# Kernel tuning notes

Hardware: AMD Instinct MI355X
Metric: run time of the kernel (lower is better)

## Reference

```python
import jax, jax.numpy as jnp
import numpy as np

V, E, H, L = 50000, 300, 256, 5
B, T_C, T_T = 64, 637, 24


def _lstm_dir(x, wih, whh, b, reverse):
    # x: [B,T,E]; wih: [4H,E]; whh: [4H,H]; b: [4H]
    pre = jnp.einsum('bte,ge->btg', x, wih) + b  # [B,T,4H]
    h0 = jnp.zeros((x.shape[0], whh.shape[1]), x.dtype)

    def step(carry, p):
        h, c = carry
        g = p + h @ whh.T
        i, f, gg, o = jnp.split(g, 4, axis=-1)
        c = jax.nn.sigmoid(f) * c + jax.nn.sigmoid(i) * jnp.tanh(gg)
        h = jax.nn.sigmoid(o) * jnp.tanh(c)
        return (h, c), h

    _, hs = jax.lax.scan(step, (h0, h0), jnp.swapaxes(pre, 0, 1), reverse=reverse)
    return jnp.swapaxes(hs, 0, 1)  # [B,T,H]


def _bilstm(x, wih_f, whh_f, b_f, wih_b, whh_b, b_b):
    return jnp.concatenate([
        _lstm_dir(x, wih_f, whh_f, b_f, False),
        _lstm_dir(x, wih_b, whh_b, b_b, True),
    ], axis=-1)  # [B,T,2H]


def setup_inputs() -> dict:
    key = jax.random.key(0)
    ks = jax.random.split(key, 20)
    k = 1.0 / np.sqrt(H)
    u = lambda kk, shape: jax.random.uniform(kk, shape, jnp.float32, -k, k)
    inp = {
        'content': jax.random.randint(ks[0], (B, T_C), 0, V),
        'title': jax.random.randint(ks[1], (B, T_T), 0, V),
        'embed_w': jax.random.normal(ks[2], (V, E), jnp.float32),
        't_wih_f': u(ks[3], (4 * H, E)), 't_whh_f': u(ks[4], (4 * H, H)), 't_b_f': u(ks[5], (4 * H,)),
        't_wih_b': u(ks[6], (4 * H, E)), 't_whh_b': u(ks[7], (4 * H, H)), 't_b_b': u(ks[8], (4 * H,)),
        'c_wih_f': u(ks[9], (4 * H, E)), 'c_whh_f': u(ks[10], (4 * H, H)), 'c_b_f': u(ks[11], (4 * H,)),
        'c_wih_b': u(ks[12], (4 * H, E)), 'c_whh_b': u(ks[13], (4 * H, H)), 'c_b_b': u(ks[14], (4 * H,)),
        'att_w': u(ks[15], (2 * H, 2 * H)),
        'fc_w': u(ks[16], (L, T_C)), 'fc_b': u(ks[17], (L,)),
    }
    return inp


def reference(content, title, embed_w, t_wih_f, t_whh_f, t_b_f, t_wih_b, t_whh_b, t_b_b,
              c_wih_f, c_whh_f, c_b_f, c_wih_b, c_whh_b, c_b_b, att_w, fc_w, fc_b):
    content_embed = embed_w[content]  # [B,Tc,E]
    title_embed = embed_w[title]      # [B,Tt,E]
    title_rep = _bilstm(title_embed, t_wih_f, t_whh_f, t_b_f, t_wih_b, t_whh_b, t_b_b)
    content_rep = _bilstm(content_embed, c_wih_f, c_whh_f, c_b_f, c_wih_b, c_whh_b, c_b_b)
    title_last = title_rep[:, -1, :]  # [B,2H]
    # score[b,t] = title_last[b] . (att_w @ content_rep[b,t])  (Linear with weight att_w: x @ att_w.T)
    a = jnp.einsum('bj,jk,btk->bt', title_last, att_w, content_rep)  # [B,Tc]
    a = jax.nn.softmax(a, axis=1)
    return jax.nn.log_softmax(a @ fc_w.T + fc_b, axis=1)  # [B,L]
```

## Files before the change

kernel.cpp:

```cpp
#include <hip/hip_runtime.h>
#include <stdint.h>

typedef __attribute__((ext_vector_type(8))) short bf16x8v;
typedef __attribute__((ext_vector_type(4))) float f32x4v;
typedef long long i64;
typedef __attribute__((ext_vector_type(2))) long long i64x2;

#define DEV static __device__ __forceinline__

#define B_   64
#define TC_  637
#define TCP_ 638
#define TT_  24
#define E_   300
#define KP_  320
#define H_   256
#define NG_  2048

DEV uint16_t f2bf(float f) {
    uint32_t u = __float_as_uint(f);
    u += 0x7fffu + ((u >> 16) & 1u);
    return (uint16_t)(u >> 16);
}
DEV float bf2f(uint16_t h) { return __uint_as_float(((uint32_t)h) << 16); }

DEV void gload_lds16(const void* g, void* l) {
    __builtin_amdgcn_global_load_lds((const __attribute__((address_space(1))) uint32_t*)g,
                                     (__attribute__((address_space(3))) uint32_t*)l, 16, 0, 0);
}

__global__ void k_pg(const float* t_wih_f, const float* t_wih_b,
                     const float* t_whh_f,
                     const float* c_wih_f, const float* c_wih_b,
                     const float* c_whh_f, const float* c_whh_b,
                     const float* t_b_f, const float* t_b_b,
                     const float* c_b_f, const float* c_b_b,
                     uint16_t* BwC, uint16_t* BwT, float* biasC, float* biasT,
                     uint32_t* w8CF, uint32_t* w8CB, uint32_t* w8TF,
                     const int* __restrict__ content, const int* __restrict__ title,
                     const float* __restrict__ emb,
                     uint16_t* __restrict__ Ac, uint16_t* __restrict__ At)
{
    if (blockIdx.x < 256) {
        int tid = blockIdx.x*blockDim.x + threadIdx.x;
        int nth = 256*256;
        for (int i = tid; i < NG_*KP_; i += nth) {
            int n = i / KP_, k = i - n*KP_;
            float vc = 0.f, vt = 0.f;
            if (k < E_) {
                vc = (n < 1024) ? c_wih_f[n*E_+k] : c_wih_b[(n-1024)*E_+k];
                vt = (n < 1024) ? t_wih_f[n*E_+k] : t_wih_b[(n-1024)*E_+k];
            }
            BwC[i] = f2bf(vc); BwT[i] = f2bf(vt);
        }
        for (int i = tid; i < 1024*H_/4; i += nth) {
            int base = i*4;
            uint32_t a, b, c;
            a = (uint32_t)__builtin_amdgcn_cvt_pk_fp8_f32(c_whh_f[base], c_whh_f[base+1], 0, false);
            a = (uint32_t)__builtin_amdgcn_cvt_pk_fp8_f32(c_whh_f[base+2], c_whh_f[base+3], (int)a, true);
            b = (uint32_t)__builtin_amdgcn_cvt_pk_fp8_f32(c_whh_b[base], c_whh_b[base+1], 0, false);
            b = (uint32_t)__builtin_amdgcn_cvt_pk_fp8_f32(c_whh_b[base+2], c_whh_b[base+3], (int)b, true);
            c = (uint32_t)__builtin_amdgcn_cvt_pk_fp8_f32(t_whh_f[base], t_whh_f[base+1], 0, false);
            c = (uint32_t)__builtin_amdgcn_cvt_pk_fp8_f32(t_whh_f[base+2], t_whh_f[base+3], (int)c, true);
            w8CF[i] = a; w8CB[i] = b; w8TF[i] = c;
        }
        for (int i = tid; i < NG_; i += nth) {
            biasC[i] = (i < 1024) ? c_b_f[i] : c_b_b[i-1024];
            biasT[i] = (i < 1024) ? t_b_f[i] : t_b_b[i-1024];
        }
    } else {
        int tid = (blockIdx.x - 256)*blockDim.x + threadIdx.x;
        int nth = 2048*256;
        const int CCH = 40832*40;
        const int TCH = 1536*40;
        for (int i = tid; i < CCH + TCH; i += nth) {
            uint16_t* dst; int row, c8; int tok;
            if (i < CCH) {
                row = i / 40; c8 = i - row*40;
                int t = row >> 6, b = row & 63;
                tok = (t < TC_) ? content[b*TC_ + t] : -1;
                dst = Ac + (size_t)row*KP_ + c8*8;
            } else {
                int jx = i - CCH;
                row = jx / 40; c8 = jx - row*40;
                int t = row >> 6, b = row & 63;
                tok = title[b*TT_ + t];
                dst = At + (size_t)row*KP_ + c8*8;
            }
            uint32_t dd[4];
            #pragma unroll
            for (int p = 0; p < 4; ++p) {
                int k = c8*8 + p*2;
                float f0 = (tok >= 0 && k   < E_) ? emb[(size_t)tok*E_ + k]   : 0.f;
                float f1 = (tok >= 0 && k+1 < E_) ? emb[(size_t)tok*E_ + k+1] : 0.f;
                dd[p] = (uint32_t)f2bf(f0) | ((uint32_t)f2bf(f1) << 16);
            }
            uint4 q; q.x = dd[0]; q.y = dd[1]; q.z = dd[2]; q.w = dd[3];
            *(uint4*)dst = q;
        }
    }
}

__global__ __launch_bounds__(256) void k_gemm(const uint16_t* __restrict__ A,
        const uint16_t* __restrict__ Bw, const float* __restrict__ bias,
        uint16_t* __restrict__ prep,
        const uint16_t* __restrict__ A2, const uint16_t* __restrict__ Bw2,
        const float* __restrict__ bias2, uint16_t* __restrict__ prep2)
{
    __shared__ __align__(16) uint16_t lA[2][128*32];
    __shared__ __align__(16) uint16_t lB[2][128*32];
    const int tid = threadIdx.x;
    const int l = tid & 63, wv = tid >> 6;

    const uint16_t* Ax; const uint16_t* Bx; const float* bx; uint16_t* px; int m0;
    if (blockIdx.y < 319) { Ax = A;  Bx = Bw;  bx = bias;  px = prep;  m0 = blockIdx.y*128; }
    else                  { Ax = A2; Bx = Bw2; bx = bias2; px = prep2; m0 = (blockIdx.y-319)*128; }
    const int n0 = blockIdx.x * 128;

    auto stage = [&](int kc, int bi) {
        #pragma unroll
        for (int r = 0; r < 2; ++r) {
            int row = r*64 + (tid >> 2);
            int cu  = (tid & 3) * 8;
            gload_lds16(Ax + (size_t)(m0 + row)*KP_ + kc*32 + cu, &lA[bi][r*2048 + wv*512]);
            gload_lds16(Bx + (size_t)(n0 + row)*KP_ + kc*32 + cu, &lB[bi][r*2048 + wv*512]);
        }
    };

    f32x4v acc[4][4];
    #pragma unroll
    for (int i = 0; i < 4; ++i)
        #pragma unroll
        for (int j = 0; j < 4; ++j)
            acc[i][j] = f32x4v{0.f,0.f,0.f,0.f};

    const int mtb = (wv >> 1) * 4, ntb = (wv & 1) * 4;

    stage(0, 0);
    __syncthreads();
    for (int kc = 0; kc < 10; ++kc) {
        if (kc < 9) stage(kc + 1, (kc + 1) & 1);
        {
            int bi = kc & 1;
            bf16x8v af[4], bfr[4];
            #pragma unroll
            for (int i = 0; i < 4; ++i) {
                af[i]  = *(const bf16x8v*)&lA[bi][((mtb+i)*16 + (l&15))*32 + (l>>4)*8];
                bfr[i] = *(const bf16x8v*)&lB[bi][((ntb+i)*16 + (l&15))*32 + (l>>4)*8];
            }
            #pragma unroll
            for (int i = 0; i < 4; ++i)
                #pragma unroll
                for (int j = 0; j < 4; ++j)
                    acc[i][j] = __builtin_amdgcn_mfma_f32_16x16x32_bf16(bfr[j], af[i], acc[i][j], 0,0,0);
        }
        __syncthreads();
    }

    const int hi = l >> 4;
    #pragma unroll
    for (int j = 0; j < 4; ++j) {
        int n16 = (n0 >> 4) + ntb + j;
        int dir = n16 >> 6;
        int q   = n16 & 63;
        int ty  = q >> 4;
        int wp  = q & 15;
        float4 bv = *(const float4*)(bx + n16*16 + hi*4);
        #pragma unroll
        for (int i = 0; i < 4; ++i) {
            int rowblk = (m0 >> 4) + mtb + i;
            int t    = rowblk >> 2;
            int bblk = rowblk & 3;
            int unit = t*8 + bblk*2 + dir;
            ushort4 pk;
            pk.x = f2bf(acc[i][j][0] + bv.x);
            pk.y = f2bf(acc[i][j][1] + bv.y);
            pk.z = f2bf(acc[i][j][2] + bv.z);
            pk.w = f2bf(acc[i][j][3] + bv.w);
            size_t off = (size_t)unit*16384 + (size_t)wp*1024 + (size_t)l*16 + ty*4;
            *(ushort4*)(px + off) = pk;
        }
    }
}

#define MF(ACC, W, AA) asm("v_mfma_f32_16x16x32_fp8_fp8 %0, %1, %2, %0" \
                           : "+v"(ACC) : "a"(W), "v"(AA))

__global__ __launch_bounds__(1024, 4) void k_rnn(
    const uint16_t* __restrict__ preC, const uint16_t* __restrict__ preT,
    const uint8_t* __restrict__ w8CF, const uint8_t* __restrict__ w8CB,
    const uint8_t* __restrict__ w8TF,
    uint16_t* __restrict__ cr, float* __restrict__ tl)
{
    __shared__ __align__(16) char smem[8192];

    const int tid = threadIdx.x;
    const int l = tid & 63, wp = tid >> 6;
    const int m = l & 15, hi = l >> 4;
    const int u = blockIdx.x;

    int dir, bblk, t0, tstep, nsteps, tlOff = -1;
    bool doCR = false;
    const uint16_t* pre; const uint8_t* whh8 = nullptr;
    if (u < 8) {
        dir = u & 1; bblk = u >> 1;
        nsteps = TC_; t0 = dir ? (TC_-1) : 0; tstep = dir ? -1 : 1;
        whh8 = dir ? w8CB : w8CF; pre = preC; doCR = true;
    } else if (u < 12) {
        dir = 0; bblk = u - 8; nsteps = TT_; t0 = 0; tstep = 1;
        whh8 = w8TF; pre = preT; tlOff = 0;
    } else {
        dir = 1; bblk = u - 12; nsteps = 1; t0 = TT_-1; tstep = -1;
        whh8 = nullptr; pre = preT; tlOff = 256;
    }
    const int b0 = bblk * 16;

    i64 w8r[4][8];
    if (whh8) {
        #pragma unroll
        for (int ty = 0; ty < 4; ++ty) {
            int n = ty*256 + wp*16 + m;
            #pragma unroll
            for (int kc = 0; kc < 8; ++kc)
                w8r[ty][kc] = *(const i64*)(whh8 + (size_t)n*H_ + kc*32 + hi*8);
        }
        #pragma unroll
        for (int ty = 0; ty < 4; ++ty)
            #pragma unroll
            for (int kc = 0; kc < 8; ++kc)
                asm volatile("" : "+a"(w8r[ty][kc]));
    }
    for (int i = tid; i < 2048; i += 1024) ((uint32_t*)smem)[i] = 0;
    __syncthreads();

    int rda[4];
    #pragma unroll
    for (int q = 0; q < 4; ++q) rda[q] = m*256 + hi*64 + (((q ^ (m & 3))) << 4);
    const int waddr = m*256 + (((wp*2 + (hi >> 1)) & 3) << 6)
                    + ((((wp >> 2) ^ (m & 3))) << 4)
                    + (((wp >> 1) & 1) << 3) + ((hi & 1) << 2);

    uint16_t* crp = cr + ((size_t)(b0 + m)*TC_ + t0)*512 + dir*256 + (wp << 4) + hi*4;
    const intptr_t crAdv = (intptr_t)tstep * 512;

    float cst[4] = {0.f, 0.f, 0.f, 0.f};

    const uint16_t* pp = pre + (size_t)(t0*8 + bblk*2 + dir)*16384
                             + (size_t)(wp << 10) + (size_t)l*16;
    const intptr_t ppAdv = (intptr_t)tstep * 131072;

    uint4 pf0 = *(const uint4*)(pp);
    uint4 pf1 = *(const uint4*)(pp + 8);

    const float KN = -1.4426950408889634f;
    const float K2 =  2.8853900817779268f;

    for (int s = 0; s < nsteps; ++s) {
        const char* hb = (const char*)smem + (s & 1)*4096;
        char*       ho = smem + ((s & 1) ^ 1)*4096;

        f32x4v acc[4];
        acc[0][0]=__uint_as_float(pf0.x<<16); acc[0][1]=__uint_as_float(pf0.x&0xffff0000u);
        acc[0][2]=__uint_as_float(pf0.y<<16); acc[0][3]=__uint_as_float(pf0.y&0xffff0000u);
        acc[1][0]=__uint_as_float(pf0.z<<16); acc[1][1]=__uint_as_float(pf0.z&0xffff0000u);
        acc[1][2]=__uint_as_float(pf0.w<<16); acc[1][3]=__uint_as_float(pf0.w&0xffff0000u);
        acc[2][0]=__uint_as_float(pf1.x<<16); acc[2][1]=__uint_as_float(pf1.x&0xffff0000u);
        acc[2][2]=__uint_as_float(pf1.y<<16); acc[2][3]=__uint_as_float(pf1.y&0xffff0000u);
        acc[3][0]=__uint_as_float(pf1.z<<16); acc[3][1]=__uint_as_float(pf1.z&0xffff0000u);
        acc[3][2]=__uint_as_float(pf1.w<<16); acc[3][3]=__uint_as_float(pf1.w&0xffff0000u);

        if (s + 1 < nsteps) {
            pp += ppAdv;
            pf0 = *(const uint4*)(pp);
            pf1 = *(const uint4*)(pp + 8);
        }

        if (whh8) {
            __builtin_amdgcn_s_setprio(1);
            #pragma unroll
            for (int q = 0; q < 4; ++q) {
                i64x2 a = *(const i64x2*)(hb + rda[q]);
                MF(acc[0], w8r[0][2*q], a[0]);
                MF(acc[1], w8r[1][2*q], a[0]);
                MF(acc[2], w8r[2][2*q], a[0]);
                MF(acc[3], w8r[3][2*q], a[0]);
                MF(acc[0], w8r[0][2*q+1], a[1]);
                MF(acc[1], w8r[1][2*q+1], a[1]);
                MF(acc[2], w8r[2][2*q+1], a[1]);
                MF(acc[3], w8r[3][2*q+1], a[1]);
            }
            __builtin_amdgcn_s_setprio(0);
        }

        float hv[4];
        #pragma unroll
        for (int r = 0; r < 4; ++r) {
            float Ei = __builtin_amdgcn_exp2f(acc[0][r] * KN);
            float Ef = __builtin_amdgcn_exp2f(acc[1][r] * KN);
            float Eg = __builtin_amdgcn_exp2f(acc[2][r] * (2.f*KN));
            float Eo = __builtin_amdgcn_exp2f(acc[3][r] * KN);
            float A  = 1.f + Ei;
            float Bb = 1.f + Eg;
            float C  = 1.f + Ef;
            float AB = A * Bb;
            float num = __builtin_fmaf(cst[r], AB, (2.f - Bb) * C);
            float cv  = num * __builtin_amdgcn_rcpf(AB * C);
            cst[r] = cv;
            float cc = fminf(fmaxf(cv, -15.f), 15.f);
            float P  = __builtin_amdgcn_exp2f(cc * K2);
            hv[r] = (P - 1.f) * __builtin_amdgcn_rcpf((1.f + Eo) * (P + 1.f));
        }

        uint32_t p8 = (uint32_t)__builtin_amdgcn_cvt_pk_fp8_f32(hv[0], hv[1], 0, false);
        p8 = (uint32_t)__builtin_amdgcn_cvt_pk_fp8_f32(hv[2], hv[3], (int)p8, true);
        *(uint32_t*)(ho + waddr) = p8;

        if (doCR) {
            uint32_t b01, b23;
            asm("v_cvt_pk_bf16_f32 %0, %1, %2" : "=v"(b01) : "v"(hv[0]), "v"(hv[1]));
            asm("v_cvt_pk_bf16_f32 %0, %1, %2" : "=v"(b23) : "v"(hv[2]), "v"(hv[3]));
            uint2 st; st.x = b01; st.y = b23;
            *(uint2*)crp = st;
            crp += crAdv;
        }
        if (tlOff >= 0 && s == nsteps - 1) {
            float4 fv; fv.x = hv[0]; fv.y = hv[1]; fv.z = hv[2]; fv.w = hv[3];
            *(float4*)(tl + (size_t)(b0 + m)*512 + tlOff + (wp << 4) + hi*4) = fv;
        }

        __builtin_amdgcn_sched_barrier(0);
        asm volatile("s_waitcnt lgkmcnt(0)" ::: "memory");
        __builtin_amdgcn_s_barrier();
        __builtin_amdgcn_sched_barrier(0);
    }
}

__global__ __launch_bounds__(256) void k_attn(const uint16_t* __restrict__ cr,
        const float* __restrict__ tl, const float* __restrict__ attw,
        const float* __restrict__ fcw, const float* __restrict__ fcb,
        float* __restrict__ out)
{
    __shared__ float sT[512];
    __shared__ float sQ[512];
    __shared__ float sS[640];
    __shared__ float sR[256];
    const int b = blockIdx.x, tid = threadIdx.x;
    for (int i = tid; i < 512; i += 256) sT[i] = tl[(size_t)b*512 + i];
    __syncthreads();
    for (int n = tid; n < 512; n += 256) {
        float s = 0.f;
        for (int j = 0; j < 512; ++j) s += sT[j] * attw[(size_t)j*512 + n];
        sQ[n] = s;
    }
    __syncthreads();
    for (int t = tid; t < TC_; t += 256) {
        const uint16_t* row = cr + ((size_t)b*TC_ + t)*512;
        float s = 0.f;
        for (int c = 0; c < 64; ++c) {
            uint4 v = *(const uint4*)(row + c*8);
            uint32_t d;
            d = v.x; s += bf2f((uint16_t)(d&0xffff))*sQ[c*8+0] + bf2f((uint16_t)(d>>16))*sQ[c*8+1];
            d = v.y; s += bf2f((uint16_t)(d&0xffff))*sQ[c*8+2] + bf2f((uint16_t)(d>>16))*sQ[c*8+3];
            d = v.z; s += bf2f((uint16_t)(d&0xffff))*sQ[c*8+4] + bf2f((uint16_t)(d>>16))*sQ[c*8+5];
            d = v.w; s += bf2f((uint16_t)(d&0xffff))*sQ[c*8+6] + bf2f((uint16_t)(d>>16))*sQ[c*8+7];
        }
        sS[t] = s;
    }
    __syncthreads();
    float lm = -1e30f;
    for (int t = tid; t < TC_; t += 256) lm = fmaxf(lm, sS[t]);
    sR[tid] = lm; __syncthreads();
    for (int o = 128; o > 0; o >>= 1) { if (tid < o) sR[tid] = fmaxf(sR[tid], sR[tid+o]); __syncthreads(); }
    float M = sR[0]; __syncthreads();
    float ls = 0.f;
    for (int t = tid; t < TC_; t += 256) { float e = __expf(sS[t]-M); sS[t] = e; ls += e; }
    sR[tid] = ls; __syncthreads();
    for (int o = 128; o > 0; o >>= 1) { if (tid < o) sR[tid] += sR[tid+o]; __syncthreads(); }
    float inv = 1.f / sR[0]; __syncthreads();
    float la[5] = {0.f,0.f,0.f,0.f,0.f};
    for (int t = tid; t < TC_; t += 256) {
        float p = sS[t] * inv;
        #pragma unroll
        for (int ll = 0; ll < 5; ++ll) la[ll] += p * fcw[ll*TC_ + t];
    }
    float lg[5];
    #pragma unroll
    for (int ll = 0; ll < 5; ++ll) {
        sR[tid] = la[ll]; __syncthreads();
        for (int o = 128; o > 0; o >>= 1) { if (tid < o) sR[tid] += sR[tid+o]; __syncthreads(); }
        lg[ll] = sR[0] + fcb[ll]; __syncthreads();
    }
    if (tid == 0) {
        float m2 = lg[0];
        #pragma unroll
        for (int ll = 1; ll < 5; ++ll) m2 = fmaxf(m2, lg[ll]);
        float se = 0.f;
        #pragma unroll
        for (int ll = 0; ll < 5; ++ll) se += __expf(lg[ll] - m2);
        float lse = __logf(se) + m2;
        #pragma unroll
        for (int ll = 0; ll < 5; ++ll) out[b*5 + ll] = lg[ll] - lse;
    }
}

extern "C" void kernel_launch(void* const* d_in, const int* in_sizes, int n_in,
                              void* d_out, int out_size, void* d_ws, size_t ws_size,
                              hipStream_t stream)
{
    const int*   content = (const int*)d_in[0];
    const int*   title   = (const int*)d_in[1];
    const float* embed_w = (const float*)d_in[2];
    const float* t_wih_f = (const float*)d_in[3];
    const float* t_whh_f = (const float*)d_in[4];
    const float* t_b_f   = (const float*)d_in[5];
    const float* t_wih_b = (const float*)d_in[6];
    const float* t_b_b   = (const float*)d_in[8];
    const float* c_wih_f = (const float*)d_in[9];
    const float* c_whh_f = (const float*)d_in[10];
    const float* c_b_f   = (const float*)d_in[11];
    const float* c_wih_b = (const float*)d_in[12];
    const float* c_whh_b = (const float*)d_in[13];
    const float* c_b_b   = (const float*)d_in[14];
    const float* att_w   = (const float*)d_in[15];
    const float* fc_w    = (const float*)d_in[16];
    const float* fc_b    = (const float*)d_in[17];
    float* out = (float*)d_out;

    char* ws = (char*)d_ws;
    size_t o = 0;
    auto alloc = [&](size_t sz) { char* p = ws + o; o = (o + sz + 255) & ~(size_t)255; return p; };
    uint16_t* Ac    = (uint16_t*)alloc((size_t)40832*KP_*2);
    uint16_t* At    = (uint16_t*)alloc((size_t)1536*KP_*2);
    uint16_t* BwC   = (uint16_t*)alloc((size_t)NG_*KP_*2);
    uint16_t* BwT   = (uint16_t*)alloc((size_t)NG_*KP_*2);
    float*    biasC = (float*)   alloc((size_t)NG_*4);
    float*    biasT = (float*)   alloc((size_t)NG_*4);
    uint8_t*  w8CF  = (uint8_t*) alloc((size_t)1024*H_);
    uint8_t*  w8CB  = (uint8_t*) alloc((size_t)1024*H_);
    uint8_t*  w8TF  = (uint8_t*) alloc((size_t)1024*H_);
    uint16_t* preC  = (uint16_t*)alloc((size_t)TCP_*262144);
    uint16_t* preT  = (uint16_t*)alloc((size_t)TT_*262144);
    uint16_t* crp   = (uint16_t*)alloc((size_t)B_*TC_*512*2);
    float*    tlp   = (float*)   alloc((size_t)B_*512*4);

    k_pg<<<2304, 256, 0, stream>>>(t_wih_f, t_wih_b, t_whh_f, c_wih_f, c_wih_b,
                                   c_whh_f, c_whh_b, t_b_f, t_b_b, c_b_f, c_b_b,
                                   BwC, BwT, biasC, biasT,
                                   (uint32_t*)w8CF, (uint32_t*)w8CB, (uint32_t*)w8TF,
                                   content, title, embed_w, Ac, At);
    k_gemm<<<dim3(16, 331), 256, 0, stream>>>(Ac, BwC, biasC, preC,
                                              At, BwT, biasT, preT);
    k_rnn<<<16, 1024, 0, stream>>>(preC, preT, w8CF, w8CB, w8TF, crp, tlp);
    k_attn<<<64, 256, 0, stream>>>(crp, tlp, att_w, fc_w, fc_b, out);
}
```

Baseline: 1.454 ms.

## Restructure LSTM recurrence to 512-thread blocks interleaving two batch chunks

```diff
diff --git a/kernel.cpp b/kernel.cpp
--- a/kernel.cpp
+++ b/kernel.cpp
@@ -164,7 +164,8 @@
         int dir = n16 >> 6;
         int q   = n16 & 63;
         int ty  = q >> 4;
-        int wp  = q & 15;
+        int wpx = q & 15;
+        int wp8 = wpx >> 1, ct = wpx & 1;
         float4 bv = *(const float4*)(bx + n16*16 + hi*4);
         #pragma unroll
         for (int i = 0; i < 4; ++i) {
@@ -177,7 +178,8 @@
             pk.y = f2bf(acc[i][j][1] + bv.y);
             pk.z = f2bf(acc[i][j][2] + bv.z);
             pk.w = f2bf(acc[i][j][3] + bv.w);
-            size_t off = (size_t)unit*16384 + (size_t)wp*1024 + (size_t)l*16 + ty*4;
+            size_t off = (size_t)unit*16384 + (size_t)wp8*2048 + (size_t)ct*1024
+                       + (size_t)l*16 + ty*4;
             *(ushort4*)(px + off) = pk;
         }
     }
@@ -186,146 +188,253 @@
 #define MF(ACC, W, AA) asm("v_mfma_f32_16x16x32_fp8_fp8 %0, %1, %2, %0" \
                            : "+v"(ACC) : "a"(W), "v"(AA))
 
-__global__ __launch_bounds__(1024, 4) void k_rnn(
+#define DEC(A0, A1, A2, A3)                                                          \
+  acc[0][0][0]=__uint_as_float(A0.x<<16); acc[0][0][1]=__uint_as_float(A0.x&0xffff0000u); \
+  acc[0][0][2]=__uint_as_float(A0.y<<16); acc[0][0][3]=__uint_as_float(A0.y&0xffff0000u); \
+  acc[1][0][0]=__uint_as_float(A0.z<<16); acc[1][0][1]=__uint_as_float(A0.z&0xffff0000u); \
+  acc[1][0][2]=__uint_as_float(A0.w<<16); acc[1][0][3]=__uint_as_float(A0.w&0xffff0000u); \
+  acc[2][0][0]=__uint_as_float(A1.x<<16); acc[2][0][1]=__uint_as_float(A1.x&0xffff0000u); \
+  acc[2][0][2]=__uint_as_float(A1.y<<16); acc[2][0][3]=__uint_as_float(A1.y&0xffff0000u); \
+  acc[3][0][0]=__uint_as_float(A1.z<<16); acc[3][0][1]=__uint_as_float(A1.z&0xffff0000u); \
+  acc[3][0][2]=__uint_as_float(A1.w<<16); acc[3][0][3]=__uint_as_float(A1.w&0xffff0000u); \
+  acc[0][1][0]=__uint_as_float(A2.x<<16); acc[0][1][1]=__uint_as_float(A2.x&0xffff0000u); \
+  acc[0][1][2]=__uint_as_float(A2.y<<16); acc[0][1][3]=__uint_as_float(A2.y&0xffff0000u); \
+  acc[1][1][0]=__uint_as_float(A2.z<<16); acc[1][1][1]=__uint_as_float(A2.z&0xffff0000u); \
+  acc[1][1][2]=__uint_as_float(A2.w<<16); acc[1][1][3]=__uint_as_float(A2.w&0xffff0000u); \
+  acc[2][1][0]=__uint_as_float(A3.x<<16); acc[2][1][1]=__uint_as_float(A3.x&0xffff0000u); \
+  acc[2][1][2]=__uint_as_float(A3.y<<16); acc[2][1][3]=__uint_as_float(A3.y&0xffff0000u); \
+  acc[3][1][0]=__uint_as_float(A3.z<<16); acc[3][1][1]=__uint_as_float(A3.z&0xffff0000u); \
+  acc[3][1][2]=__uint_as_float(A3.w<<16); acc[3][1][3]=__uint_as_float(A3.w&0xffff0000u);
+
+#define MFMA_BLOCK(HB)                                     \
+  __builtin_amdgcn_s_setprio(1);                           \
+  _Pragma("unroll")                                        \
+  for (int q = 0; q < 4; ++q) {                            \
+    i64x2 a = *(const i64x2*)((HB) + rda[q]);              \
+    MF(acc[0][0], w8r[0][0][2*q], a[0]);                   \
+    MF(acc[1][0], w8r[1][0][2*q], a[0]);                   \
+    MF(acc[2][0], w8r[2][0][2*q], a[0]);                   \
+    MF(acc[3][0], w8r[3][0][2*q], a[0]);                   \
+    MF(acc[0][1], w8r[0][1][2*q], a[0]);                   \
+    MF(acc[1][1], w8r[1][1][2*q], a[0]);                   \
+    MF(acc[2][1], w8r[2][1][2*q], a[0]);                   \
+    MF(acc[3][1], w8r[3][1][2*q], a[0]);                   \
+    MF(acc[0][0], w8r[0][0][2*q+1], a[1]);                 \
+    MF(acc[1][0], w8r[1][0][2*q+1], a[1]);                 \
+    MF(acc[2][0], w8r[2][0][2*q+1], a[1]);                 \
+    MF(acc[3][0], w8r[3][0][2*q+1], a[1]);                 \
+    MF(acc[0][1], w8r[0][1][2*q+1], a[1]);                 \
+    MF(acc[1][1], w8r[1][1][2*q+1], a[1]);                 \
+    MF(acc[2][1], w8r[2][1][2*q+1], a[1]);                 \
+    MF(acc[3][1], w8r[3][1][2*q+1], a[1]);                 \
+  }                                                        \
+  __builtin_amdgcn_s_setprio(0);
+
+#define NL(CT, CS, HV)                                                          \
+  _Pragma("unroll")                                                             \
+  for (int r = 0; r < 4; ++r) {                                                 \
+    float Ei = __builtin_amdgcn_exp2f(acc[0][CT][r] * KN);                      \
+    float Ef = __builtin_amdgcn_exp2f(acc[1][CT][r] * KN);                      \
+    float Eg = __builtin_amdgcn_exp2f(acc[2][CT][r] * (2.f*KN));                \
+    float Eo = __builtin_amdgcn_exp2f(acc[3][CT][r] * KN);                      \
+    float Av = 1.f + Ei, Bb = 1.f + Eg, Cv = 1.f + Ef;                          \
+    float AB = Av * Bb;                                                         \
+    float num = __builtin_fmaf(CS[r], AB, (2.f - Bb) * Cv);                     \
+    float cv  = num * __builtin_amdgcn_rcpf(AB * Cv);                           \
+    CS[r] = cv;                                                                 \
+    float cc = fminf(fmaxf(cv, -15.f), 15.f);                                   \
+    float P  = __builtin_amdgcn_exp2f(cc * K2);                                 \
+    HV[r] = (P - 1.f) * __builtin_amdgcn_rcpf((1.f + Eo) * (P + 1.f));          \
+  }
+
+__global__ __launch_bounds__(512, 2) void k_rnn(
     const uint16_t* __restrict__ preC, const uint16_t* __restrict__ preT,
     const uint8_t* __restrict__ w8CF, const uint8_t* __restrict__ w8CB,
     const uint8_t* __restrict__ w8TF,
     uint16_t* __restrict__ cr, float* __restrict__ tl)
 {
-    __shared__ __align__(16) char smem[8192];
+    __shared__ __align__(16) char smem[16384];
 
     const int tid = threadIdx.x;
-    const int l = tid & 63, wp = tid >> 6;
+    const int l = tid & 63, wp8 = tid >> 6;
     const int m = l & 15, hi = l >> 4;
     const int u = blockIdx.x;
 
-    int dir, bblk, t0, tstep, nsteps, tlOff = -1;
-    bool doCR = false;
-    const uint16_t* pre; const uint8_t* whh8 = nullptr;
-    if (u < 8) {
-        dir = u & 1; bblk = u >> 1;
-        nsteps = TC_; t0 = dir ? (TC_-1) : 0; tstep = dir ? -1 : 1;
-        whh8 = dir ? w8CB : w8CF; pre = preC; doCR = true;
-    } else if (u < 12) {
-        dir = 0; bblk = u - 8; nsteps = TT_; t0 = 0; tstep = 1;
-        whh8 = w8TF; pre = preT; tlOff = 0;
+    const float KN = -1.4426950408889634f;
+    const float K2 =  2.8853900817779268f;
+
+    if (u == 6) {
+        for (int chunk = 0; chunk < 4; ++chunk) {
+            const uint16_t* pp = preT + (size_t)((TT_-1)*8 + chunk*2 + 1)*16384
+                               + (size_t)wp8*2048 + (size_t)l*16;
+            uint4 p0 = *(const uint4*)(pp);
+            uint4 p1 = *(const uint4*)(pp + 8);
+            uint4 p2 = *(const uint4*)(pp + 1024);
+            uint4 p3 = *(const uint4*)(pp + 1032);
+            f32x4v acc[4][2];
+            DEC(p0, p1, p2, p3);
+            float cz0[4] = {0,0,0,0}, cz1[4] = {0,0,0,0};
+            float hv0[4], hv1[4];
+            NL(0, cz0, hv0);
+            NL(1, cz1, hv1);
+            float* tb = tl + (size_t)(chunk*16 + m)*512 + 256 + wp8*32 + hi*4;
+            float4 f0; f0.x=hv0[0]; f0.y=hv0[1]; f0.z=hv0[2]; f0.w=hv0[3];
+            float4 f1; f1.x=hv1[0]; f1.y=hv1[1]; f1.z=hv1[2]; f1.w=hv1[3];
+            *(float4*)tb = f0;
+            *(float4*)(tb + 16) = f1;
+        }
+        return;
+    }
+
+    int dir, nsteps, t0, tstep, tlOff, chunkA, chunkB;
+    bool doCR;
+    const uint16_t* pre; const uint8_t* whh8;
+    if (u < 4) {
+        dir = u >> 1; int pr = u & 1;
+        chunkA = pr*2; chunkB = pr*2 + 1;
+        nsteps = TC_; t0 = dir ? TC_-1 : 0; tstep = dir ? -1 : 1;
+        whh8 = dir ? w8CB : w8CF; pre = preC; doCR = true; tlOff = -1;
     } else {
-        dir = 1; bblk = u - 12; nsteps = 1; t0 = TT_-1; tstep = -1;
-        whh8 = nullptr; pre = preT; tlOff = 256;
-    }
-    const int b0 = bblk * 16;
-
-    i64 w8r[4][8];
-    if (whh8) {
-        #pragma unroll
-        for (int ty = 0; ty < 4; ++ty) {
-            int n = ty*256 + wp*16 + m;
+        dir = 0; int pr = u - 4;
+        chunkA = pr*2; chunkB = pr*2 + 1;
+        nsteps = TT_; t0 = 0; tstep = 1;
+        whh8 = w8TF; pre = preT; doCR = false; tlOff = 0;
+    }
+
+    i64 w8r[4][2][8];
+    #pragma unroll
+    for (int ty = 0; ty < 4; ++ty)
+        #pragma unroll
+        for (int ct = 0; ct < 2; ++ct) {
+            int n = ty*256 + wp8*32 + ct*16 + m;
             #pragma unroll
             for (int kc = 0; kc < 8; ++kc)
-                w8r[ty][kc] = *(const i64*)(whh8 + (size_t)n*H_ + kc*32 + hi*8);
-        }
-        #pragma unroll
-        for (int ty = 0; ty < 4; ++ty)
+                w8r[ty][ct][kc] = *(const i64*)(whh8 + (size_t)n*H_ + kc*32 + hi*8);
+        }
+    #pragma unroll
+    for (int ty = 0; ty < 4; ++ty)
+        #pragma unroll
+        for (int ct = 0; ct < 2; ++ct)
             #pragma unroll
             for (int kc = 0; kc < 8; ++kc)
-                asm volatile("" : "+a"(w8r[ty][kc]));
-    }
-    for (int i = tid; i < 2048; i += 1024) ((uint32_t*)smem)[i] = 0;
+                asm volatile("" : "+a"(w8r[ty][ct][kc]));
+
+    for (int i = tid; i < 4096; i += 512) ((uint32_t*)smem)[i] = 0;
     __syncthreads();
 
     int rda[4];
     #pragma unroll
-    for (int q = 0; q < 4; ++q) rda[q] = m*256 + hi*64 + (((q ^ (m & 3))) << 4);
-    const int waddr = m*256 + (((wp*2 + (hi >> 1)) & 3) << 6)
-                    + ((((wp >> 2) ^ (m & 3))) << 4)
-                    + (((wp >> 1) & 1) << 3) + ((hi & 1) << 2);
-
-    uint16_t* crp = cr + ((size_t)(b0 + m)*TC_ + t0)*512 + dir*256 + (wp << 4) + hi*4;
+    for (int q = 0; q < 4; ++q) rda[q] = m*256 + hi*64 + ((q ^ (m & 3)) << 4);
+    auto WAD = [&](int wpx) {
+        return m*256 + (((wpx*2 + (hi >> 1)) & 3) << 6)
+             + (((wpx >> 2) ^ (m & 3)) << 4)
+             + (((wpx >> 1) & 1) << 3) + ((hi & 1) << 2);
+    };
+    const int wA0 = WAD(wp8*2), wA1 = WAD(wp8*2 + 1);
+
+    uint16_t* crpA = cr + ((size_t)(chunkA*16 + m)*TC_ + t0)*512 + dir*256 + wp8*32 + hi*4;
+    uint16_t* crpB = cr + ((size_t)(chunkB*16 + m)*TC_ + t0)*512 + dir*256 + wp8*32 + hi*4;
     const intptr_t crAdv = (intptr_t)tstep * 512;
 
-    float cst[4] = {0.f, 0.f, 0.f, 0.f};
-
-    const uint16_t* pp = pre + (size_t)(t0*8 + bblk*2 + dir)*16384
-                             + (size_t)(wp << 10) + (size_t)l*16;
+    float cstA[2][4] = {{0,0,0,0},{0,0,0,0}};
+    float cstB[2][4] = {{0,0,0,0},{0,0,0,0}};
+
+    const uint16_t* ppA = pre + (size_t)(t0*8 + chunkA*2 + dir)*16384
+                        + (size_t)wp8*2048 + (size_t)l*16;
+    const uint16_t* ppB = pre + (size_t)(t0*8 + chunkB*2 + dir)*16384
+                        + (size_t)wp8*2048 + (size_t)l*16;
     const intptr_t ppAdv = (intptr_t)tstep * 131072;
 
-    uint4 pf0 = *(const uint4*)(pp);
-    uint4 pf1 = *(const uint4*)(pp + 8);
-
-    const float KN = -1.4426950408889634f;
-    const float K2 =  2.8853900817779268f;
+    uint4 pf0 = *(const uint4*)(ppA);
+    uint4 pf1 = *(const uint4*)(ppA + 8);
+    uint4 pf2 = *(const uint4*)(ppA + 1024);
+    uint4 pf3 = *(const uint4*)(ppA + 1032);
 
     for (int s = 0; s < nsteps; ++s) {
-        const char* hb = (const char*)smem + (s & 1)*4096;
-        char*       ho = smem + ((s & 1) ^ 1)*4096;
-
-        f32x4v acc[4];
-        acc[0][0]=__uint_as_float(pf0.x<<16); acc[0][1]=__uint_as_float(pf0.x&0xffff0000u);
-        acc[0][2]=__uint_as_float(pf0.y<<16); acc[0][3]=__uint_as_float(pf0.y&0xffff0000u);
-        acc[1][0]=__uint_as_float(pf0.z<<16); acc[1][1]=__uint_as_float(pf0.z&0xffff0000u);
-        acc[1][2]=__uint_as_float(pf0.w<<16); acc[1][3]=__uint_as_float(pf0.w&0xffff0000u);
-        acc[2][0]=__uint_as_float(pf1.x<<16); acc[2][1]=__uint_as_float(pf1.x&0xffff0000u);
-        acc[2][2]=__uint_as_float(pf1.y<<16); acc[2][3]=__uint_as_float(pf1.y&0xffff0000u);
-        acc[3][0]=__uint_as_float(pf1.z<<16); acc[3][1]=__uint_as_float(pf1.z&0xffff0000u);
-        acc[3][2]=__uint_as_float(pf1.w<<16); acc[3][3]=__uint_as_float(pf1.w&0xffff0000u);
-
-        if (s + 1 < nsteps) {
-            pp += ppAdv;
-            pf0 = *(const uint4*)(pp);
-            pf1 = *(const uint4*)(pp + 8);
-        }
-
-        if (whh8) {
-            __builtin_amdgcn_s_setprio(1);
-            #pragma unroll
-            for (int q = 0; q < 4; ++q) {
-                i64x2 a = *(const i64x2*)(hb + rda[q]);
-                MF(acc[0], w8r[0][2*q], a[0]);
-                MF(acc[1], w8r[1][2*q], a[0]);
-                MF(acc[2], w8r[2][2*q], a[0]);
-                MF(acc[3], w8r[3][2*q], a[0]);
-                MF(acc[0], w8r[0][2*q+1], a[1]);
-                MF(acc[1], w8r[1][2*q+1], a[1]);
-                MF(acc[2], w8r[2][2*q+1], a[1]);
-                MF(acc[3], w8r[3][2*q+1], a[1]);
-            }
-            __builtin_amdgcn_s_setprio(0);
-        }
-
-        float hv[4];
-        #pragma unroll
-        for (int r = 0; r < 4; ++r) {
-            float Ei = __builtin_amdgcn_exp2f(acc[0][r] * KN);
-            float Ef = __builtin_amdgcn_exp2f(acc[1][r] * KN);
-            float Eg = __builtin_amdgcn_exp2f(acc[2][r] * (2.f*KN));
-            float Eo = __builtin_amdgcn_exp2f(acc[3][r] * KN);
-            float A  = 1.f + Ei;
-            float Bb = 1.f + Eg;
-            float C  = 1.f + Ef;
-            float AB = A * Bb;
-            float num = __builtin_fmaf(cst[r], AB, (2.f - Bb) * C);
-            float cv  = num * __builtin_amdgcn_rcpf(AB * C);
-            cst[r] = cv;
-            float cc = fminf(fmaxf(cv, -15.f), 15.f);
-            float P  = __builtin_amdgcn_exp2f(cc * K2);
-            hv[r] = (P - 1.f) * __builtin_amdgcn_rcpf((1.f + Eo) * (P + 1.f));
-        }
-
-        uint32_t p8 = (uint32_t)__builtin_amdgcn_cvt_pk_fp8_f32(hv[0], hv[1], 0, false);
-        p8 = (uint32_t)__builtin_amdgcn_cvt_pk_fp8_f32(hv[2], hv[3], (int)p8, true);
-        *(uint32_t*)(ho + waddr) = p8;
-
-        if (doCR) {
-            uint32_t b01, b23;
-            asm("v_cvt_pk_bf16_f32 %0, %1, %2" : "=v"(b01) : "v"(hv[0]), "v"(hv[1]));
-            asm("v_cvt_pk_bf16_f32 %0, %1, %2" : "=v"(b23) : "v"(hv[2]), "v"(hv[3]));
-            uint2 st; st.x = b01; st.y = b23;
-            *(uint2*)crp = st;
-            crp += crAdv;
-        }
-        if (tlOff >= 0 && s == nsteps - 1) {
-            float4 fv; fv.x = hv[0]; fv.y = hv[1]; fv.z = hv[2]; fv.w = hv[3];
-            *(float4*)(tl + (size_t)(b0 + m)*512 + tlOff + (wp << 4) + hi*4) = fv;
+        const int rb = (s & 1)*4096, wb = ((s & 1) ^ 1)*4096;
+        const bool last = (s == nsteps - 1);
+
+        f32x4v acc[4][2];
+        DEC(pf0, pf1, pf2, pf3);
+        pf0 = *(const uint4*)(ppB);
+        pf1 = *(const uint4*)(ppB + 8);
+        pf2 = *(const uint4*)(ppB + 1024);
+        pf3 = *(const uint4*)(ppB + 1032);
+
+        MFMA_BLOCK(smem + rb)
+
+        {
+            float hv0[4], hv1[4];
+            NL(0, cstA[0], hv0);
+            NL(1, cstA[1], hv1);
+            uint32_t a8 = (uint32_t)__builtin_amdgcn_cvt_pk_fp8_f32(hv0[0], hv0[1], 0, false);
+            a8 = (uint32_t)__builtin_amdgcn_cvt_pk_fp8_f32(hv0[2], hv0[3], (int)a8, true);
+            uint32_t b8 = (uint32_t)__builtin_amdgcn_cvt_pk_fp8_f32(hv1[0], hv1[1], 0, false);
+            b8 = (uint32_t)__builtin_amdgcn_cvt_pk_fp8_f32(hv1[2], hv1[3], (int)b8, true);
+            *(uint32_t*)(smem + wb + wA0) = a8;
+            *(uint32_t*)(smem + wb + wA1) = b8;
+            if (doCR) {
+                uint32_t c01, c23, d01, d23;
+                asm("v_cvt_pk_bf16_f32 %0, %1, %2" : "=v"(c01) : "v"(hv0[0]), "v"(hv0[1]));
+                asm("v_cvt_pk_bf16_f32 %0, %1, %2" : "=v"(c23) : "v"(hv0[2]), "v"(hv0[3]));
+                asm("v_cvt_pk_bf16_f32 %0, %1, %2" : "=v"(d01) : "v"(hv1[0]), "v"(hv1[1]));
+                asm("v_cvt_pk_bf16_f32 %0, %1, %2" : "=v"(d23) : "v"(hv1[2]), "v"(hv1[3]));
+                uint2 s0; s0.x = c01; s0.y = c23;
+                uint2 s1; s1.x = d01; s1.y = d23;
+                *(uint2*)crpA = s0;
+                *(uint2*)(crpA + 16) = s1;
+                crpA += crAdv;
+            }
+            if (tlOff >= 0 && last) {
+                float* tb = tl + (size_t)(chunkA*16 + m)*512 + tlOff + wp8*32 + hi*4;
+                float4 f0; f0.x=hv0[0]; f0.y=hv0[1]; f0.z=hv0[2]; f0.w=hv0[3];
+                float4 f1; f1.x=hv1[0]; f1.y=hv1[1]; f1.z=hv1[2]; f1.w=hv1[3];
+                *(float4*)tb = f0;
+                *(float4*)(tb + 16) = f1;
+            }
+        }
+
+        DEC(pf0, pf1, pf2, pf3);
+        if (!last) {
+            ppA += ppAdv;
+            pf0 = *(const uint4*)(ppA);
+            pf1 = *(const uint4*)(ppA + 8);
+            pf2 = *(const uint4*)(ppA + 1024);
+            pf3 = *(const uint4*)(ppA + 1032);
+        }
+
+        MFMA_BLOCK(smem + 8192 + rb)
+
+        {
+            float hv0[4], hv1[4];
+            NL(0, cstB[0], hv0);
+            NL(1, cstB[1], hv1);
+            uint32_t a8 = (uint32_t)__builtin_amdgcn_cvt_pk_fp8_f32(hv0[0], hv0[1], 0, false);
+            a8 = (uint32_t)__builtin_amdgcn_cvt_pk_fp8_f32(hv0[2], hv0[3], (int)a8, true);
+            uint32_t b8 = (uint32_t)__builtin_amdgcn_cvt_pk_fp8_f32(hv1[0], hv1[1], 0, false);
+            b8 = (uint32_t)__builtin_amdgcn_cvt_pk_fp8_f32(hv1[2], hv1[3], (int)b8, true);
+            *(uint32_t*)(smem + 8192 + wb + wA0) = a8;
+            *(uint32_t*)(smem + 8192 + wb + wA1) = b8;
+            if (doCR) {
+                uint32_t c01, c23, d01, d23;
+                asm("v_cvt_pk_bf16_f32 %0, %1, %2" : "=v"(c01) : "v"(hv0[0]), "v"(hv0[1]));
+                asm("v_cvt_pk_bf16_f32 %0, %1, %2" : "=v"(c23) : "v"(hv0[2]), "v"(hv0[3]));
+                asm("v_cvt_pk_bf16_f32 %0, %1, %2" : "=v"(d01) : "v"(hv1[0]), "v"(hv1[1]));
+                asm("v_cvt_pk_bf16_f32 %0, %1, %2" : "=v"(d23) : "v"(hv1[2]), "v"(hv1[3]));
+                uint2 s0; s0.x = c01; s0.y = c23;
+                uint2 s1; s1.x = d01; s1.y = d23;
+                *(uint2*)crpB = s0;
+                *(uint2*)(crpB + 16) = s1;
+                crpB += crAdv;
+            }
+            if (tlOff >= 0 && last) {
+                float* tb = tl + (size_t)(chunkB*16 + m)*512 + tlOff + wp8*32 + hi*4;
+                float4 f0; f0.x=hv0[0]; f0.y=hv0[1]; f0.z=hv0[2]; f0.w=hv0[3];
+                float4 f1; f1.x=hv1[0]; f1.y=hv1[1]; f1.z=hv1[2]; f1.w=hv1[3];
+                *(float4*)tb = f0;
+                *(float4*)(tb + 16) = f1;
+            }
+            if (!last) ppB += ppAdv;
         }
 
         __builtin_amdgcn_sched_barrier(0);
@@ -450,6 +559,6 @@
                                    content, title, embed_w, Ac, At);
     k_gemm<<<dim3(16, 331), 256, 0, stream>>>(Ac, BwC, biasC, preC,
                                               At, BwT, biasT, preT);
-    k_rnn<<<16, 1024, 0, stream>>>(preC, preT, w8CF, w8CB, w8TF, crp, tlp);
+    k_rnn<<<7, 512, 0, stream>>>(preC, preT, w8CF, w8CB, w8TF, crp, tlp);
     k_attn<<<64, 256, 0, stream>>>(crp, tlp, att_w, fc_w, fc_b, out);
 }
```

Measured after the change: 2.879 ms. +98.0%, slower.
